# Kernel optimization log

Hardware: AMD Instinct MI355X
Metric: run time of the kernel (lower is better)

Reference implementation:

```python
import jax, jax.numpy as jnp
import numpy as np

N_HEADS = 16


def apply_rotary_emb(x, cos, sin):
    # x: [B, H, S, hd]; cos/sin: [S, hd//2] (broadcast over B, H)
    xr = x.reshape(x.shape[:-1] + (-1, 2))
    r, i = xr[..., 0], xr[..., 1]
    a = r * cos - i * sin
    b = i * cos + r * sin
    return jnp.stack([a, b], axis=-1).reshape(x.shape).astype(x.dtype)


def setup_inputs() -> dict:
    key = jax.random.key(0)
    ks = jax.random.split(key, 7)
    B, S, D = 2, 2048, 1024
    hd = D // N_HEADS
    x = jax.random.normal(ks[0], (B, S, D), dtype=jnp.float32)
    freqs_cos = jax.random.uniform(ks[1], (S, hd // 2), dtype=jnp.float32)
    freqs_sin = jax.random.uniform(ks[2], (S, hd // 2), dtype=jnp.float32)
    sc = 1.0 / np.sqrt(D)
    Wq = jax.random.normal(ks[3], (D, D), dtype=jnp.float32) * sc
    Wk = jax.random.normal(ks[4], (D, D), dtype=jnp.float32) * sc
    Wv = jax.random.normal(ks[5], (D, D), dtype=jnp.float32) * sc
    Wo = jax.random.normal(ks[6], (D, D), dtype=jnp.float32) * sc
    return {"x": x, "freqs_cos": freqs_cos, "freqs_sin": freqs_sin,
            "Wq": Wq, "Wk": Wk, "Wv": Wv, "Wo": Wo}


def reference(x, freqs_cos, freqs_sin, Wq, Wk, Wv, Wo):
    B, S, D = x.shape
    H = N_HEADS
    hd = D // H
    # QKV projections (nn.Linear: x @ W.T)
    q = (x @ Wq.T).reshape(B, S, H, hd).transpose(0, 2, 1, 3)
    k = (x @ Wk.T).reshape(B, S, H, hd).transpose(0, 2, 1, 3)
    v = (x @ Wv.T).reshape(B, S, H, hd).transpose(0, 2, 1, 3)
    q = apply_rotary_emb(q, freqs_cos, freqs_sin)
    k = apply_rotary_emb(k, freqs_cos, freqs_sin)
    # causal SDPA (scale = 1/sqrt(head_dim), as in F.scaled_dot_product_attention)
    scores = jnp.einsum("bhqd,bhkd->bhqk", q, k) * (1.0 / np.sqrt(hd))
    causal = jnp.tril(jnp.ones((S, S), dtype=bool))
    scores = jnp.where(causal, scores, -jnp.inf)
    probs = jax.nn.softmax(scores, axis=-1)
    attn_out = jnp.einsum("bhqk,bhkd->bhqd", probs, v)
    attn_cat = attn_out.transpose(0, 2, 1, 3).reshape(B, S, D)
    return attn_cat @ Wo.T
```

## Files before the change

### kernel.cpp

```cpp
#include <hip/hip_runtime.h>
#include <hip/hip_bf16.h>
#include <cstdint>

typedef __attribute__((ext_vector_type(8))) short short8;
typedef __attribute__((ext_vector_type(4))) float f32x4;

#define B_  2
#define S_  2048
#define D_  1024
#define H_  16
#define HD  64

static __device__ __forceinline__ float bf2f(unsigned int u16) {
    union { unsigned int i; float f; } v; v.i = u16 << 16; return v.f;
}
static __device__ __forceinline__ unsigned short f2bf(float f) {
    union { float f; unsigned int i; } v; v.f = f;
    unsigned int r = v.i + 0x7FFFu + ((v.i >> 16) & 1u);
    return (unsigned short)(r >> 16);
}
static __device__ __forceinline__ unsigned pack_bf16(float hi, float lo) {
    union { float f; unsigned u; } h, l;
    h.f = hi; l.f = lo;
    return __builtin_amdgcn_perm(h.u + 0x8000u, l.u + 0x8000u, 0x07060302);
}
static __device__ __forceinline__ void load_lds_16B(const unsigned short* g, unsigned short* l) {
    __builtin_amdgcn_global_load_lds(
        (const __attribute__((address_space(1))) unsigned int*)g,
        (__attribute__((address_space(3))) unsigned int*)l, 16, 0, 0);
}

__global__ void cvt_f32_bf16(const float* __restrict__ src,
                             unsigned short* __restrict__ dst, int n4) {
    int i = blockIdx.x * 256 + threadIdx.x;
    if (i >= n4) return;
    float4 f = ((const float4*)src)[i];
    uint2 o;
    o.x = (unsigned int)f2bf(f.x) | ((unsigned int)f2bf(f.y) << 16);
    o.y = (unsigned int)f2bf(f.z) | ((unsigned int)f2bf(f.w) << 16);
    ((uint2*)dst)[i] = o;
}

__global__ void cvt_w4(const float* __restrict__ w0, const float* __restrict__ w1,
                       const float* __restrict__ w2, const float* __restrict__ w3,
                       unsigned short* __restrict__ dst) {
    int bid = blockIdx.x;
    int wsel = bid >> 10;
    const float* s = wsel == 0 ? w0 : wsel == 1 ? w1 : wsel == 2 ? w2 : w3;
    int i = (bid & 1023) * 256 + threadIdx.x;
    float4 f = ((const float4*)s)[i];
    uint2 o;
    o.x = (unsigned int)f2bf(f.x) | ((unsigned int)f2bf(f.y) << 16);
    o.y = (unsigned int)f2bf(f.z) | ((unsigned int)f2bf(f.w) << 16);
    ((uint2*)dst)[(size_t)wsel * 262144 + i] = o;
}

__global__ __launch_bounds__(256) void qkv_gemm(
    const unsigned short* __restrict__ xbf,
    const unsigned short* __restrict__ wq,
    const unsigned short* __restrict__ wk,
    const unsigned short* __restrict__ wv,
    unsigned short* __restrict__ qb,
    unsigned short* __restrict__ kb,
    unsigned short* __restrict__ vb)
{
    __shared__ unsigned short As[128 * 32];
    __shared__ unsigned short Bs[128 * 32];

    const int tid  = threadIdx.x;
    const int w    = tid >> 6, lane = tid & 63;
    const int l15  = lane & 15, quad = lane >> 4;
    const int wrow = (w >> 1) * 64, wcol = (w & 1) * 64;

    const int m0 = blockIdx.x * 128;
    const int nc = blockIdx.y * 128;
    const int sel = nc >> 10;
    const int n0 = nc & 1023;
    const unsigned short* __restrict__ W = sel == 0 ? wq : (sel == 1 ? wk : wv);
    unsigned short* __restrict__ Out = sel == 0 ? qb : (sel == 1 ? kb : vb);

    const int lr = lane >> 2, lc = (lane & 3) * 8;
    const unsigned short* ga = xbf + (size_t)(m0 + w * 16 + lr) * 1024 + lc;
    const unsigned short* gb = W   + (size_t)(n0 + w * 16 + lr) * 1024 + lc;
    unsigned short* la0 = As + (w * 16) * 32;
    unsigned short* la1 = As + (64 + w * 16) * 32;
    unsigned short* lb0 = Bs + (w * 16) * 32;
    unsigned short* lb1 = Bs + (64 + w * 16) * 32;

    f32x4 acc[4][4] = {};

    for (int k0 = 0; k0 < 1024; k0 += 32) {
        __syncthreads();
        load_lds_16B(ga + k0,             la0);
        load_lds_16B(ga + 64 * 1024 + k0, la1);
        load_lds_16B(gb + k0,             lb0);
        load_lds_16B(gb + 64 * 1024 + k0, lb1);
        __syncthreads();

        short8 a[4], b[4];
#pragma unroll
        for (int i = 0; i < 4; i++)
            a[i] = *(const short8*)&As[(wrow + i * 16 + l15) * 32 + quad * 8];
#pragma unroll
        for (int j = 0; j < 4; j++)
            b[j] = *(const short8*)&Bs[(wcol + j * 16 + l15) * 32 + quad * 8];
#pragma unroll
        for (int i = 0; i < 4; i++)
#pragma unroll
            for (int j = 0; j < 4; j++)
                acc[i][j] = __builtin_amdgcn_mfma_f32_16x16x32_bf16(a[i], b[j], acc[i][j], 0, 0, 0);
    }

#pragma unroll
    for (int i = 0; i < 4; i++) {
#pragma unroll
        for (int r = 0; r < 4; r++) {
            int m = m0 + wrow + i * 16 + quad * 4 + r;
            int bb = m >> 11, s = m & 2047;
#pragma unroll
            for (int j = 0; j < 4; j++) {
                int n = n0 + wcol + j * 16 + l15;
                int h = n >> 6, d = n & 63;
                Out[(((size_t)(bb * H_ + h) * S_) + s) * HD + d] = f2bf(acc[i][j][r]);
            }
        }
    }
}

__global__ __launch_bounds__(256) void out_gemm(
    const unsigned short* __restrict__ A,
    const unsigned short* __restrict__ Bt,
    float* __restrict__ C)
{
    __shared__ unsigned short As[128 * 32];
    __shared__ unsigned short Bs[128 * 32];

    const int tid  = threadIdx.x;
    const int w    = tid >> 6, lane = tid & 63;
    const int l15  = lane & 15, quad = lane >> 4;
    const int wrow = (w >> 1) * 64, wcol = (w & 1) * 64;

    const int m0 = blockIdx.x * 128;
    const int n0 = blockIdx.y * 128;

    const int lr = lane >> 2, lc = (lane & 3) * 8;
    const unsigned short* ga = A  + (size_t)(m0 + w * 16 + lr) * 1024 + lc;
    const unsigned short* gb = Bt + (size_t)(n0 + w * 16 + lr) * 1024 + lc;
    unsigned short* la0 = As + (w * 16) * 32;
    unsigned short* la1 = As + (64 + w * 16) * 32;
    unsigned short* lb0 = Bs + (w * 16) * 32;
    unsigned short* lb1 = Bs + (64 + w * 16) * 32;

    f32x4 acc[4][4] = {};

    for (int k0 = 0; k0 < 1024; k0 += 32) {
        __syncthreads();
        load_lds_16B(ga + k0,             la0);
        load_lds_16B(ga + 64 * 1024 + k0, la1);
        load_lds_16B(gb + k0,             lb0);
        load_lds_16B(gb + 64 * 1024 + k0, lb1);
        __syncthreads();

        short8 a[4], b[4];
#pragma unroll
        for (int i = 0; i < 4; i++)
            a[i] = *(const short8*)&As[(wrow + i * 16 + l15) * 32 + quad * 8];
#pragma unroll
        for (int j = 0; j < 4; j++)
            b[j] = *(const short8*)&Bs[(wcol + j * 16 + l15) * 32 + quad * 8];
#pragma unroll
        for (int i = 0; i < 4; i++)
#pragma unroll
            for (int j = 0; j < 4; j++)
                acc[i][j] = __builtin_amdgcn_mfma_f32_16x16x32_bf16(a[i], b[j], acc[i][j], 0, 0, 0);
    }

#pragma unroll
    for (int i = 0; i < 4; i++)
#pragma unroll
        for (int r = 0; r < 4; r++) {
            int m = m0 + wrow + i * 16 + quad * 4 + r;
#pragma unroll
            for (int j = 0; j < 4; j++)
                C[(size_t)m * 1024 + n0 + wcol + j * 16 + l15] = acc[i][j][r];
        }
}

__global__ void rope_qk(unsigned short* __restrict__ qb,
                        unsigned short* __restrict__ kb,
                        const float* __restrict__ fcos,
                        const float* __restrict__ fsin)
{
    const float SCQ = 0.125f * 1.44269504f;
    int idx = blockIdx.x * 256 + threadIdx.x;
    int t  = idx & 31;
    int s  = (idx >> 5) & (S_ - 1);
    int bh = idx >> 16;
    float c  = fcos[s * 32 + t];
    float si = fsin[s * 32 + t];
    float cq = c * SCQ, sq = si * SCQ;
    size_t off = ((size_t)bh * S_ + s) * HD + 2 * t;

    unsigned int* qp = (unsigned int*)(qb + off);
    unsigned int u = *qp;
    float r = bf2f(u & 0xffffu), im = bf2f(u >> 16);
    *qp = pack_bf16(im * cq + r * sq, r * cq - im * sq);

    unsigned int* kp = (unsigned int*)(kb + off);
    u = *kp;
    r = bf2f(u & 0xffffu); im = bf2f(u >> 16);
    *kp = pack_bf16(im * c + r * si, r * c - im * si);
}

__global__ __launch_bounds__(256) void v_transpose(
    const unsigned short* __restrict__ vb,
    unsigned short* __restrict__ vT)
{
    __shared__ unsigned short T[64][72];
    const int bh = blockIdx.x;
    const int j0 = blockIdx.y * 64;
    const int tid = threadIdx.x;
    const int vdg = tid >> 5, vp = tid & 31;
    const unsigned short* vptr = vb + ((size_t)bh * S_ + j0 + 2 * vp) * HD + vdg * 8;
    uint4 v0 = *(const uint4*)vptr;
    uint4 v1 = *(const uint4*)(vptr + HD);
    const unsigned* a0 = (const unsigned*)&v0;
    const unsigned* a1 = (const unsigned*)&v1;
#pragma unroll
    for (int c = 0; c < 4; c++) {
        *(unsigned*)&T[vdg * 8 + 2 * c][2 * vp]     = __builtin_amdgcn_perm(a1[c], a0[c], 0x05040100);
        *(unsigned*)&T[vdg * 8 + 2 * c + 1][2 * vp] = __builtin_amdgcn_perm(a1[c], a0[c], 0x07060302);
    }
    __syncthreads();
    const int d = tid >> 3, js = (tid & 7) * 8;
#pragma unroll
    for (int dd = 0; dd < 2; dd++) {
        short8 row = *(const short8*)&T[dd * 32 + d][js];
        *(short8*)(vT + ((size_t)bh * HD + dd * 32 + d) * S_ + j0 + js) = row;
    }
}

__global__ __launch_bounds__(256) void flash_attn_mfma(
    const unsigned short* __restrict__ qb,
    const unsigned short* __restrict__ kb,
    const unsigned short* __restrict__ vT,
    unsigned short* __restrict__ attnc)
{
    __shared__ __attribute__((aligned(1024))) unsigned short Ks[2][2][64][32];
    __shared__ __attribute__((aligned(1024))) unsigned short Vt[64][64];
    __shared__ unsigned short Pls[4][16][72];

    const int bh   = blockIdx.x;
    const int qtb  = blockIdx.y;
    const int jj = qtb & 7, mm = qtb >> 3;
    const int qt = (mm == 0) ? jj : (mm == 1) ? 31 - jj : (mm == 2) ? 8 + jj : 23 - jj;

    const int b    = bh >> 4, h = bh & 15;
    const int tid  = threadIdx.x;
    const int w    = tid >> 6;
    const int lane = tid & 63;
    const int l15  = lane & 15;
    const int quad = lane >> 4;

    const size_t bhS = (size_t)bh * S_;
    const unsigned short* __restrict__ vTb = vT + (size_t)bh * HD * S_;

    short8 qfrag[2];
    {
        const unsigned short* qp = qb + (bhS + qt * 64 + w * 16 + l15) * HD + quad * 8;
        qfrag[0] = *(const short8*)(qp);
        qfrag[1] = *(const short8*)(qp + 32);
    }

    const int ksrow  = lane >> 2;
    const int ksslot = (lane & 3) ^ ((lane >> 3) & 3);
    const int vsrow  = lane >> 3;
    const int vsslot = (lane & 7) ^ vsrow;

    const int ckq = (quad ^ ((l15 >> 1) & 3)) << 4;
    const int s7  = l15 & 7;

    f32x4 O[4] = {};
    float mrow = -INFINITY;
    float lrow = 0.0f;

    auto STAGE_K = [&](int jt, int bufi) {
        const int j0 = jt * 64;
        const unsigned short* kg = kb + (bhS + j0 + w * 16 + ksrow) * HD + ksslot * 8;
        load_lds_16B(kg,      &Ks[bufi][0][w * 16][0]);
        load_lds_16B(kg + 32, &Ks[bufi][1][w * 16][0]);
    };
    auto STAGE_V = [&](int jt) {
        const int j0 = jt * 64;
        const unsigned short* vg = vTb + (size_t)(w * 16 + vsrow) * S_ + j0 + vsslot * 8;
        load_lds_16B(vg,          &Vt[w * 16][0]);
        load_lds_16B(vg + 8 * S_, &Vt[w * 16 + 8][0]);
    };

    STAGE_K(0, 0);

    for (int jt = 0; jt <= qt; jt++) {
        const int cur = jt & 1;
        if (jt < qt) {
            STAGE_K(jt + 1, cur ^ 1);
            STAGE_V(jt);
            asm volatile("s_waitcnt vmcnt(4)" ::: "memory");
        } else {
            STAGE_V(jt);
            asm volatile("s_waitcnt vmcnt(2)" ::: "memory");
        }
        __builtin_amdgcn_s_barrier();

        const bool diag  = (jt == qt);
        const int  nsub  = diag ? (w + 1) : 4;
        const int  kgmax = (nsub + 1) >> 1;

        f32x4 Sacc[4];
        float tmax = -INFINITY;
        for (int sub = 0; sub < nsub; sub++) {
            f32x4 s = {};
#pragma unroll
            for (int kh = 0; kh < 2; kh++) {
                int bo = ((sub * 16 + l15) << 6) + ckq;
                short8 kf = *(const short8*)((const char*)&Ks[cur][kh][0][0] + bo);
                s = __builtin_amdgcn_mfma_f32_16x16x32_bf16(kf, qfrag[kh], s, 0, 0, 0);
            }
#pragma unroll
            for (int r = 0; r < 4; r++) {
                float v = s[r];
                if (diag && (sub * 16 + quad * 4 + r > w * 16 + l15)) v = -INFINITY;
                s[r] = v;
                tmax = fmaxf(tmax, v);
            }
            Sacc[sub] = s;
        }
        tmax = fmaxf(tmax, __shfl_xor(tmax, 16, 64));
        tmax = fmaxf(tmax, __shfl_xor(tmax, 32, 64));

        if (__any(tmax > mrow + 8.0f)) {
            float mnew = fmaxf(mrow, tmax);
            float ccr  = __builtin_amdgcn_exp2f(mrow - mnew);
            lrow *= ccr;
#pragma unroll
            for (int r = 0; r < 4; r++) {
                float ccq = __shfl(ccr, quad * 4 + r, 64);
#pragma unroll
                for (int dt = 0; dt < 4; dt++) O[dt][r] *= ccq;
            }
            mrow = mnew;
        }

        float psum = 0.0f;
        for (int sub = 0; sub < nsub; sub++) {
            f32x4 s = Sacc[sub];
            float p0 = __builtin_amdgcn_exp2f(s[0] - mrow);
            float p1 = __builtin_amdgcn_exp2f(s[1] - mrow);
            float p2 = __builtin_amdgcn_exp2f(s[2] - mrow);
            float p3 = __builtin_amdgcn_exp2f(s[3] - mrow);
            psum += (p0 + p1) + (p2 + p3);
            uint2 pk;
            pk.x = pack_bf16(p1, p0);
            pk.y = pack_bf16(p3, p2);
            *(uint2*)&Pls[w][l15][sub * 16 + quad * 4] = pk;
        }
        if (diag) {
            for (int sub = nsub; sub < 2 * kgmax; sub++) {
                uint2 z; z.x = 0u; z.y = 0u;
                *(uint2*)&Pls[w][l15][sub * 16 + quad * 4] = z;
            }
        }
        psum += __shfl_xor(psum, 16, 64);
        psum += __shfl_xor(psum, 32, 64);
        lrow += psum;

        if (jt < qt) {
            asm volatile("s_waitcnt vmcnt(2)" ::: "memory");
        } else {
            asm volatile("s_waitcnt vmcnt(0)" ::: "memory");
        }
        __builtin_amdgcn_s_barrier();

        for (int kg = 0; kg < kgmax; kg++) {
            short8 pf = *(const short8*)&Pls[w][l15][kg * 32 + quad * 8];
#pragma unroll
            for (int dt = 0; dt < 4; dt++) {
                int row = dt * 16 + l15;
                int slot = (((kg << 2) | quad) ^ s7) << 4;
                short8 vf = *(const short8*)((const char*)&Vt[0][0] + (row << 7) + slot);
                O[dt] = __builtin_amdgcn_mfma_f32_16x16x32_bf16(pf, vf, O[dt], 0, 0, 0);
            }
        }

        asm volatile("" ::: "memory");
        __builtin_amdgcn_s_barrier();
    }

    float inv = 1.0f / lrow;
#pragma unroll
    for (int r = 0; r < 4; r++) {
        float invq = __shfl(inv, quad * 4 + r, 64);
        int qabs = qt * 64 + w * 16 + quad * 4 + r;
        unsigned short* op = attnc + (((size_t)b * S_ + qabs) * H_ + h) * HD + l15;
#pragma unroll
        for (int dt = 0; dt < 4; dt++)
            op[dt * 16] = f2bf(O[dt][r] * invq);
    }
}

extern "C" void kernel_launch(void* const* d_in, const int* in_sizes, int n_in,
                              void* d_out, int out_size, void* d_ws, size_t ws_size,
                              hipStream_t stream) {
    const float* x    = (const float*)d_in[0];
    const float* fcos = (const float*)d_in[1];
    const float* fsin = (const float*)d_in[2];
    const float* Wq   = (const float*)d_in[3];
    const float* Wk   = (const float*)d_in[4];
    const float* Wv   = (const float*)d_in[5];
    const float* Wo   = (const float*)d_in[6];
    float* out = (float*)d_out;

    unsigned short* ws = (unsigned short*)d_ws;
    unsigned short* xbf = ws;
    unsigned short* wqb = xbf + 4096 * 1024;
    unsigned short* wkb = wqb + 1024 * 1024;
    unsigned short* wvb = wkb + 1024 * 1024;
    unsigned short* wob = wvb + 1024 * 1024;
    unsigned short* qb  = wob + 1024 * 1024;
    unsigned short* kb  = qb + 4096 * 1024;
    unsigned short* vb  = kb + 4096 * 1024;
    unsigned short* attnc = vb + 4096 * 1024;
    unsigned short* vT = xbf;

    cvt_f32_bf16<<<4096, 256, 0, stream>>>(x, xbf, 4096 * 1024 / 4);
    cvt_w4<<<4096, 256, 0, stream>>>(Wq, Wk, Wv, Wo, wqb);

    qkv_gemm<<<dim3(32, 24), 256, 0, stream>>>(xbf, wqb, wkb, wvb, qb, kb, vb);

    v_transpose<<<dim3(32, 32), 256, 0, stream>>>(vb, vT);

    rope_qk<<<8192, 256, 0, stream>>>(qb, kb, fcos, fsin);

    flash_attn_mfma<<<dim3(32, 32), 256, 0, stream>>>(qb, kb, vT, attnc);

    out_gemm<<<dim3(32, 8), 256, 0, stream>>>(attnc, wob, out);
}
```

Before: 218.8 us.

## Fuse RoPE and V transpose into QKV GEMM epilogue, merge conversions, MFMA row sums

Merges the x and weight f32->bf16 conversion kernels into one launch. RoPE and the softmax scale are now applied inside the QKV GEMM epilogue, with a lane shuffle to pair real and imaginary parts, and V is written directly in transposed layout. This removes the separate rope and v_transpose kernels along with their global round trips. In flash attention, the softmax denominator is now accumulated with an extra MFMA against a ones vector instead of shuffle reductions. The costs are strided 2-byte scattered stores for V^T, per-element cos/sin loads in the epilogue, and a row sum built from bf16-rounded probabilities.

```diff
diff --git a/kernel.cpp b/kernel.cpp
--- a/kernel.cpp
+++ b/kernel.cpp
@@ -30,29 +30,30 @@
         (__attribute__((address_space(3))) unsigned int*)l, 16, 0, 0);
 }
 
-__global__ void cvt_f32_bf16(const float* __restrict__ src,
-                             unsigned short* __restrict__ dst, int n4) {
-    int i = blockIdx.x * 256 + threadIdx.x;
-    if (i >= n4) return;
-    float4 f = ((const float4*)src)[i];
-    uint2 o;
-    o.x = (unsigned int)f2bf(f.x) | ((unsigned int)f2bf(f.y) << 16);
-    o.y = (unsigned int)f2bf(f.z) | ((unsigned int)f2bf(f.w) << 16);
-    ((uint2*)dst)[i] = o;
-}
-
-__global__ void cvt_w4(const float* __restrict__ w0, const float* __restrict__ w1,
-                       const float* __restrict__ w2, const float* __restrict__ w3,
-                       unsigned short* __restrict__ dst) {
+__global__ void cvt_all(const float* __restrict__ x,
+                        const float* __restrict__ w0, const float* __restrict__ w1,
+                        const float* __restrict__ w2, const float* __restrict__ w3,
+                        unsigned short* __restrict__ xbf,
+                        unsigned short* __restrict__ wdst) {
     int bid = blockIdx.x;
-    int wsel = bid >> 10;
-    const float* s = wsel == 0 ? w0 : wsel == 1 ? w1 : wsel == 2 ? w2 : w3;
-    int i = (bid & 1023) * 256 + threadIdx.x;
-    float4 f = ((const float4*)s)[i];
-    uint2 o;
-    o.x = (unsigned int)f2bf(f.x) | ((unsigned int)f2bf(f.y) << 16);
-    o.y = (unsigned int)f2bf(f.z) | ((unsigned int)f2bf(f.w) << 16);
-    ((uint2*)dst)[(size_t)wsel * 262144 + i] = o;
+    if (bid < 4096) {
+        int i = bid * 256 + threadIdx.x;
+        float4 f = ((const float4*)x)[i];
+        uint2 o;
+        o.x = (unsigned int)f2bf(f.x) | ((unsigned int)f2bf(f.y) << 16);
+        o.y = (unsigned int)f2bf(f.z) | ((unsigned int)f2bf(f.w) << 16);
+        ((uint2*)xbf)[i] = o;
+    } else {
+        int wb = bid - 4096;
+        int wsel = wb >> 10;
+        const float* s = wsel == 0 ? w0 : wsel == 1 ? w1 : wsel == 2 ? w2 : w3;
+        int i = (wb & 1023) * 256 + threadIdx.x;
+        float4 f = ((const float4*)s)[i];
+        uint2 o;
+        o.x = (unsigned int)f2bf(f.x) | ((unsigned int)f2bf(f.y) << 16);
+        o.y = (unsigned int)f2bf(f.z) | ((unsigned int)f2bf(f.w) << 16);
+        ((uint2*)wdst)[(size_t)wsel * 262144 + i] = o;
+    }
 }
 
 __global__ __launch_bounds__(256) void qkv_gemm(
@@ -60,6 +61,8 @@
     const unsigned short* __restrict__ wq,
     const unsigned short* __restrict__ wk,
     const unsigned short* __restrict__ wv,
+    const float* __restrict__ fcos,
+    const float* __restrict__ fsin,
     unsigned short* __restrict__ qb,
     unsigned short* __restrict__ kb,
     unsigned short* __restrict__ vb)
@@ -77,7 +80,6 @@
     const int sel = nc >> 10;
     const int n0 = nc & 1023;
     const unsigned short* __restrict__ W = sel == 0 ? wq : (sel == 1 ? wk : wv);
-    unsigned short* __restrict__ Out = sel == 0 ? qb : (sel == 1 ? kb : vb);
 
     const int lr = lane >> 2, lc = (lane & 3) * 8;
     const unsigned short* ga = xbf + (size_t)(m0 + w * 16 + lr) * 1024 + lc;
@@ -111,19 +113,43 @@
                 acc[i][j] = __builtin_amdgcn_mfma_f32_16x16x32_bf16(a[i], b[j], acc[i][j], 0, 0, 0);
     }
 
-#pragma unroll
-    for (int i = 0; i < 4; i++) {
-#pragma unroll
-        for (int r = 0; r < 4; r++) {
-            int m = m0 + wrow + i * 16 + quad * 4 + r;
-            int bb = m >> 11, s = m & 2047;
-#pragma unroll
-            for (int j = 0; j < 4; j++) {
-                int n = n0 + wcol + j * 16 + l15;
-                int h = n >> 6, d = n & 63;
-                Out[(((size_t)(bb * H_ + h) * S_) + s) * HD + d] = f2bf(acc[i][j][r]);
-            }
-        }
+    if (sel == 2) {
+#pragma unroll
+        for (int i = 0; i < 4; i++)
+#pragma unroll
+            for (int r = 0; r < 4; r++) {
+                int m = m0 + wrow + i * 16 + quad * 4 + r;
+                int bb = m >> 11, s = m & 2047;
+#pragma unroll
+                for (int j = 0; j < 4; j++) {
+                    int n = n0 + wcol + j * 16 + l15;
+                    int h = n >> 6, d = n & 63;
+                    vb[(((size_t)(bb * H_ + h)) * HD + d) * S_ + s] = f2bf(acc[i][j][r]);
+                }
+            }
+    } else {
+        unsigned short* __restrict__ Out = sel == 0 ? qb : kb;
+        const float qsc = (sel == 0) ? 0.125f * 1.44269504f : 1.0f;
+        const int odd = l15 & 1;
+#pragma unroll
+        for (int i = 0; i < 4; i++)
+#pragma unroll
+            for (int r = 0; r < 4; r++) {
+                int m = m0 + wrow + i * 16 + quad * 4 + r;
+                int bb = m >> 11, s = m & 2047;
+#pragma unroll
+                for (int j = 0; j < 4; j++) {
+                    int n = n0 + wcol + j * 16 + l15;
+                    int h = n >> 6, d = n & 63;
+                    int t = d >> 1;
+                    float c  = fcos[s * 32 + t];
+                    float si = fsin[s * 32 + t];
+                    float own = acc[i][j][r];
+                    float oth = __shfl_xor(own, 1, 64);
+                    float outv = odd ? (own * c + oth * si) : (own * c - oth * si);
+                    Out[(((size_t)(bb * H_ + h) * S_) + s) * HD + d] = f2bf(outv * qsc);
+                }
+            }
     }
 }
 
@@ -184,60 +210,6 @@
             for (int j = 0; j < 4; j++)
                 C[(size_t)m * 1024 + n0 + wcol + j * 16 + l15] = acc[i][j][r];
         }
-}
-
-__global__ void rope_qk(unsigned short* __restrict__ qb,
-                        unsigned short* __restrict__ kb,
-                        const float* __restrict__ fcos,
-                        const float* __restrict__ fsin)
-{
-    const float SCQ = 0.125f * 1.44269504f;
-    int idx = blockIdx.x * 256 + threadIdx.x;
-    int t  = idx & 31;
-    int s  = (idx >> 5) & (S_ - 1);
-    int bh = idx >> 16;
-    float c  = fcos[s * 32 + t];
-    float si = fsin[s * 32 + t];
-    float cq = c * SCQ, sq = si * SCQ;
-    size_t off = ((size_t)bh * S_ + s) * HD + 2 * t;
-
-    unsigned int* qp = (unsigned int*)(qb + off);
-    unsigned int u = *qp;
-    float r = bf2f(u & 0xffffu), im = bf2f(u >> 16);
-    *qp = pack_bf16(im * cq + r * sq, r * cq - im * sq);
-
-    unsigned int* kp = (unsigned int*)(kb + off);
-    u = *kp;
-    r = bf2f(u & 0xffffu); im = bf2f(u >> 16);
-    *kp = pack_bf16(im * c + r * si, r * c - im * si);
-}
-
-__global__ __launch_bounds__(256) void v_transpose(
-    const unsigned short* __restrict__ vb,
-    unsigned short* __restrict__ vT)
-{
-    __shared__ unsigned short T[64][72];
-    const int bh = blockIdx.x;
-    const int j0 = blockIdx.y * 64;
-    const int tid = threadIdx.x;
-    const int vdg = tid >> 5, vp = tid & 31;
-    const unsigned short* vptr = vb + ((size_t)bh * S_ + j0 + 2 * vp) * HD + vdg * 8;
-    uint4 v0 = *(const uint4*)vptr;
-    uint4 v1 = *(const uint4*)(vptr + HD);
-    const unsigned* a0 = (const unsigned*)&v0;
-    const unsigned* a1 = (const unsigned*)&v1;
-#pragma unroll
-    for (int c = 0; c < 4; c++) {
-        *(unsigned*)&T[vdg * 8 + 2 * c][2 * vp]     = __builtin_amdgcn_perm(a1[c], a0[c], 0x05040100);
-        *(unsigned*)&T[vdg * 8 + 2 * c + 1][2 * vp] = __builtin_amdgcn_perm(a1[c], a0[c], 0x07060302);
-    }
-    __syncthreads();
-    const int d = tid >> 3, js = (tid & 7) * 8;
-#pragma unroll
-    for (int dd = 0; dd < 2; dd++) {
-        short8 row = *(const short8*)&T[dd * 32 + d][js];
-        *(short8*)(vT + ((size_t)bh * HD + dd * 32 + d) * S_ + j0 + js) = row;
-    }
 }
 
 __global__ __launch_bounds__(256) void flash_attn_mfma(
@@ -280,9 +252,13 @@
     const int ckq = (quad ^ ((l15 >> 1) & 3)) << 4;
     const int s7  = l15 & 7;
 
+    short8 ones;
+#pragma unroll
+    for (int i = 0; i < 8; i++) ones[i] = (short)0x3F80;
+
     f32x4 O[4] = {};
+    f32x4 Osum = {};
     float mrow = -INFINITY;
-    float lrow = 0.0f;
 
     auto STAGE_K = [&](int jt, int bufi) {
         const int j0 = jt * 64;
@@ -340,24 +316,22 @@
         if (__any(tmax > mrow + 8.0f)) {
             float mnew = fmaxf(mrow, tmax);
             float ccr  = __builtin_amdgcn_exp2f(mrow - mnew);
-            lrow *= ccr;
 #pragma unroll
             for (int r = 0; r < 4; r++) {
                 float ccq = __shfl(ccr, quad * 4 + r, 64);
 #pragma unroll
                 for (int dt = 0; dt < 4; dt++) O[dt][r] *= ccq;
+                Osum[r] *= ccq;
             }
             mrow = mnew;
         }
 
-        float psum = 0.0f;
         for (int sub = 0; sub < nsub; sub++) {
             f32x4 s = Sacc[sub];
             float p0 = __builtin_amdgcn_exp2f(s[0] - mrow);
             float p1 = __builtin_amdgcn_exp2f(s[1] - mrow);
             float p2 = __builtin_amdgcn_exp2f(s[2] - mrow);
             float p3 = __builtin_amdgcn_exp2f(s[3] - mrow);
-            psum += (p0 + p1) + (p2 + p3);
             uint2 pk;
             pk.x = pack_bf16(p1, p0);
             pk.y = pack_bf16(p3, p2);
@@ -369,9 +343,6 @@
                 *(uint2*)&Pls[w][l15][sub * 16 + quad * 4] = z;
             }
         }
-        psum += __shfl_xor(psum, 16, 64);
-        psum += __shfl_xor(psum, 32, 64);
-        lrow += psum;
 
         if (jt < qt) {
             asm volatile("s_waitcnt vmcnt(2)" ::: "memory");
@@ -389,16 +360,16 @@
                 short8 vf = *(const short8*)((const char*)&Vt[0][0] + (row << 7) + slot);
                 O[dt] = __builtin_amdgcn_mfma_f32_16x16x32_bf16(pf, vf, O[dt], 0, 0, 0);
             }
+            Osum = __builtin_amdgcn_mfma_f32_16x16x32_bf16(pf, ones, Osum, 0, 0, 0);
         }
 
         asm volatile("" ::: "memory");
         __builtin_amdgcn_s_barrier();
     }
 
-    float inv = 1.0f / lrow;
 #pragma unroll
     for (int r = 0; r < 4; r++) {
-        float invq = __shfl(inv, quad * 4 + r, 64);
+        float invq = 1.0f / Osum[r];
         int qabs = qt * 64 + w * 16 + quad * 4 + r;
         unsigned short* op = attnc + (((size_t)b * S_ + qabs) * H_ + h) * HD + l15;
 #pragma unroll
@@ -429,18 +400,12 @@
     unsigned short* kb  = qb + 4096 * 1024;
     unsigned short* vb  = kb + 4096 * 1024;
     unsigned short* attnc = vb + 4096 * 1024;
-    unsigned short* vT = xbf;
-
-    cvt_f32_bf16<<<4096, 256, 0, stream>>>(x, xbf, 4096 * 1024 / 4);
-    cvt_w4<<<4096, 256, 0, stream>>>(Wq, Wk, Wv, Wo, wqb);
-
-    qkv_gemm<<<dim3(32, 24), 256, 0, stream>>>(xbf, wqb, wkb, wvb, qb, kb, vb);
-
-    v_transpose<<<dim3(32, 32), 256, 0, stream>>>(vb, vT);
-
-    rope_qk<<<8192, 256, 0, stream>>>(qb, kb, fcos, fsin);
-
-    flash_attn_mfma<<<dim3(32, 32), 256, 0, stream>>>(qb, kb, vT, attnc);
+
+    cvt_all<<<8192, 256, 0, stream>>>(x, Wq, Wk, Wv, Wo, xbf, wqb);
+
+    qkv_gemm<<<dim3(32, 24), 256, 0, stream>>>(xbf, wqb, wkb, wvb, fcos, fsin, qb, kb, vb);
+
+    flash_attn_mfma<<<dim3(32, 32), 256, 0, stream>>>(qb, kb, vb, attnc);
 
     out_gemm<<<dim3(32, 8), 256, 0, stream>>>(attnc, wob, out);
 }
```

Measured after the change: 219.6 us. Within noise of the previous version (+0.4%).
